# Optimization experiments

Measured on AMD Instinct MI355X. Metric: run time of the kernel, lower is better.

Reference implementation:

```python
import jax, jax.numpy as jnp
import numpy as np

DT = 0.02        # time step
DT_SKIP = DT * 20
ITERS = 49       # BDF2 iterations hardcoded in forward()
P = 64           # tronc (reduced dim)
NG_U = 8000      # HR sample count, u-equation
NG_V = 8000      # HR sample count, v-equation
B = 32           # batch of trajectories


def setup_inputs() -> dict:
    key = jax.random.key(0)
    k0, k1, k2, k3, k4 = jax.random.split(key, 5)
    state = jax.random.normal(k0, (B, P), dtype=jnp.float32)
    Ap = jax.random.normal(k1, (P, P), dtype=jnp.float32) * 0.05
    W_all_u = jax.random.normal(k2, (4 * NG_U, P), dtype=jnp.float32) * 0.02
    W_all_v = jax.random.normal(k3, (4 * NG_V, P), dtype=jnp.float32) * 0.02
    P_proj = jax.random.normal(k4, (P, NG_U + NG_V), dtype=jnp.float32) * 0.02
    return {"state": state, "Ap": Ap, "W_all_u": W_all_u,
            "W_all_v": W_all_v, "P_proj": P_proj}


def _rhs(a, W_all_u, W_all_v, P_proj):
    # a: (B, p) -> (B, p). Batched hyper-reduced quadratic RHS.
    zu = a @ W_all_u.T                       # (B, 4*Ng_u)
    uu, vu, dxu, dyu = jnp.split(zu, 4, axis=1)
    fu = uu * dxu + vu * dyu                 # (B, Ng_u)
    zv = a @ W_all_v.T                       # (B, 4*Ng_v)
    uv, vv, dxv, dyv = jnp.split(zv, 4, axis=1)
    fv = uv * dxv + vv * dyv                 # (B, Ng_v)
    concat = jnp.concatenate([fu, fv], axis=1)  # (B, Ng_u+Ng_v)
    return -(concat @ P_proj.T)              # (B, p)


def reference(state, Ap, W_all_u, W_all_v, P_proj):
    dt = jnp.float32(DT)
    a0 = state[:, :P]                        # state_rom (B, p)
    eye = jnp.eye(P, dtype=state.dtype)
    mat_1st = eye - dt * Ap[:P, :P]          # I - dt*A
    mat_2nd = 3.0 * eye - 2.0 * dt * Ap[:P, :P]

    # first step: implicit Euler
    f0 = _rhs(a0, W_all_u, W_all_v, P_proj)
    r0 = a0 + dt * f0
    a1 = jnp.linalg.solve(mat_1st, r0.T).T   # == lu_solve(LU_1st, ...)

    # BDF2 recurrence
    def step(carry, _):
        a_prev, f_prev, a_new = carry
        f_new = _rhs(a_new, W_all_u, W_all_v, P_proj)
        r = 4.0 * a_new - a_prev + 4.0 * dt * f_new - 2.0 * dt * f_prev
        a_next = jnp.linalg.solve(mat_2nd, r.T).T
        return (a_new, f_new, a_next), None

    (_, _, out_new), _ = jax.lax.scan(step, (a0, f0, a1), None, length=ITERS)
    return (out_new - a0) / jnp.float32(DT_SKIP)
```

## Files before the change

kernel.cpp:

```cpp
#include <hip/hip_runtime.h>

#define DTC 0.02f
#define INV_DT_SKIP 2.5f
#define NBLK 32
#define NSTEP 50

typedef __attribute__((ext_vector_type(8))) __bf16 bf16x8;
typedef __attribute__((ext_vector_type(4))) float f32x4;
typedef __attribute__((ext_vector_type(8))) unsigned short us8;
typedef unsigned long long u64t;

__device__ inline unsigned short f2bf(float x) {
    unsigned u = __float_as_uint(x);
    unsigned r = u + 0x7FFF + ((u >> 16) & 1u);
    return (unsigned short)(r >> 16);
}
__device__ inline float bf2f(unsigned short h) {
    return __uint_as_float(((unsigned)h) << 16);
}
__device__ inline unsigned pack2(float a, float b) {
    return (unsigned)f2bf(a) | ((unsigned)f2bf(b) << 16);
}
__device__ inline void gstore32(unsigned* p, unsigned v) {
    __hip_atomic_store(p, v, __ATOMIC_RELAXED, __HIP_MEMORY_SCOPE_AGENT);
}
__device__ inline u64t gload64(const u64t* p) {
    return __hip_atomic_load(p, __ATOMIC_RELAXED, __HIP_MEMORY_SCOPE_AGENT);
}

__global__ __launch_bounds__(256) void kinv(const float* __restrict__ Ap,
                                            float* __restrict__ inv1,
                                            float* __restrict__ inv2) {
    const int t = threadIdx.x;
    const float coef  = (blockIdx.x == 0) ? DTC : (2.0f * DTC / 3.0f);
    const float scale = (blockIdx.x == 0) ? 1.0f : (1.0f / 3.0f);
    float* outp = (blockIdx.x == 0) ? inv1 : inv2;

    __shared__ float ET[64 * 68];
    __shared__ float XA[64 * 68];
    __shared__ float XB[64 * 68];

    for (int idx = t; idx < 4096; idx += 256) {
        int r = idx >> 6, c = idx & 63;
        float e = coef * Ap[idx];
        ET[c * 68 + r] = e;
        XA[r * 68 + c] = ((r == c) ? 1.0f : 0.0f) + e;
    }
    __syncthreads();

    const int rr = (t >> 4) << 2;
    const int cc = (t & 15) << 2;
    float* bufs[2] = {XA, XB};
    for (int it = 0; it < 3; it++) {
        const float* Xin = bufs[it & 1];
        float* Xout = bufs[(it + 1) & 1];
        float acc[4][4];
        #pragma unroll
        for (int i = 0; i < 4; i++)
            #pragma unroll
            for (int j = 0; j < 4; j++)
                acc[i][j] = ((rr + i) == (cc + j)) ? 1.0f : 0.0f;
        for (int k = 0; k < 64; k++) {
            float4 e4 = *(const float4*)&ET[k * 68 + rr];
            float4 x4 = *(const float4*)&Xin[k * 68 + cc];
            float ev[4] = {e4.x, e4.y, e4.z, e4.w};
            float xv[4] = {x4.x, x4.y, x4.z, x4.w};
            #pragma unroll
            for (int i = 0; i < 4; i++)
                #pragma unroll
                for (int j = 0; j < 4; j++)
                    acc[i][j] += ev[i] * xv[j];
        }
        __syncthreads();
        #pragma unroll
        for (int i = 0; i < 4; i++)
            #pragma unroll
            for (int j = 0; j < 4; j++)
                Xout[(rr + i) * 68 + cc + j] = acc[i][j];
        __syncthreads();
    }
    const float* Xf = bufs[1];
    for (int idx = t; idx < 4096; idx += 256) {
        int r = idx >> 6, c = idx & 63;
        outp[idx] = scale * Xf[r * 68 + c];
    }
}

__global__ void kzero(unsigned* __restrict__ flags) {
    if (threadIdx.x < NBLK) flags[threadIdx.x] = 0u;
}

__device__ inline void flagbar(unsigned* flags, int blk, unsigned target) {
    __syncthreads();
    if (threadIdx.x < 64) {
        if (threadIdx.x == 0)
            __hip_atomic_store(&flags[blk], target, __ATOMIC_RELEASE, __HIP_MEMORY_SCOPE_AGENT);
        for (;;) {
            unsigned v = __hip_atomic_load(&flags[threadIdx.x & (NBLK - 1)], __ATOMIC_ACQUIRE,
                                           __HIP_MEMORY_SCOPE_AGENT);
            if (__all(v >= target)) break;
            __builtin_amdgcn_s_sleep(2);
        }
    }
    __syncthreads();
}

__global__ __launch_bounds__(512, 2)
void kmain(const float* __restrict__ state,
           const float* __restrict__ Wu,
           const float* __restrict__ Wv,
           const float* __restrict__ Pp,
           const float* __restrict__ inv1,
           const float* __restrict__ inv2,
           unsigned* __restrict__ pbuf,
           unsigned* __restrict__ flags,
           float* __restrict__ out) {
    const int t = threadIdx.x;
    const int l = t & 63;
    const int w = t >> 6;
    const int blk = blockIdx.x;
    const int gw = blk * 8 + w;
    const bool active = (gw < 250);

    __shared__ float Ab[3][2176];
    __shared__ float fb[8][16][36];
    __shared__ float red[8][1024];
    __shared__ float rbuf[32 * 68];

    for (int i = t; i < 2048; i += 512) Ab[0][(i >> 6) * 68 + (i & 63)] = state[i];
    if (!active)
        for (int i = l; i < 1024; i += 64) red[w][i] = 0.f;

    const int nr = l & 15;
    const int c0 = (l >> 4) << 3;
    const int cA = gw * 2;
    const float* W = (cA < 250) ? Wu : Wv;
    const int glA = ((cA < 250) ? cA : cA - 250) * 32;

    bf16x8 wf[2][2][4][2], pf[2][4], sfw[2];
    if (active) {
        #pragma unroll
        for (int ch = 0; ch < 2; ch++)
            #pragma unroll
            for (int th = 0; th < 2; th++)
                #pragma unroll
                for (int rb = 0; rb < 4; rb++)
                    #pragma unroll
                    for (int kt = 0; kt < 2; kt++) {
                        const float* s = W + (size_t)(rb * 8000 + glA + ch * 32 + th * 16 + nr) * 64
                                           + kt * 32 + c0;
                        us8 o;
                        #pragma unroll
                        for (int j = 0; j < 8; j++) o[j] = f2bf(s[j]);
                        wf[ch][th][rb][kt] = __builtin_bit_cast(bf16x8, o);
                    }
        #pragma unroll
        for (int ch = 0; ch < 2; ch++)
            #pragma unroll
            for (int pt = 0; pt < 4; pt++) {
                const float* s = Pp + (size_t)(pt * 16 + nr) * 16000 + (cA + ch) * 32 + c0;
                us8 o;
                #pragma unroll
                for (int j = 0; j < 8; j++) o[j] = f2bf(s[j]);
                pf[ch][pt] = __builtin_bit_cast(bf16x8, o);
            }
    }
    {
        const int ptS = w & 3;
        #pragma unroll
        for (int kt = 0; kt < 2; kt++) {
            int p = ptS * 16 + nr;
            const float* s = inv2 + (size_t)p * 64 + kt * 32 + c0;
            us8 o;
            #pragma unroll
            for (int j = 0; j < 8; j++) {
                float v = s[j] - ((p == kt * 32 + c0 + j) ? (1.0f / 3.0f) : 0.0f);
                o[j] = f2bf(v);
            }
            sfw[kt] = __builtin_bit_cast(bf16x8, o);
        }
    }
    __syncthreads();

    int ia_prev = 2, ia_cur = 0, ia_next = 1;
    float fprev[4];

    for (int k = 0; k < NSTEP; k++) {
        const int par = k & 1;
        unsigned* pslot = pbuf + (size_t)par * (NBLK * 1024) + blk * 1024;

        #pragma unroll
        for (int mt = 0; mt < 2; mt++) {
            if (active) {
                bf16x8 ahi[2], alo[2];
                {
                    const float* ac = Ab[ia_cur];
                    #pragma unroll
                    for (int kt = 0; kt < 2; kt++) {
                        us8 hv, lv;
                        #pragma unroll
                        for (int j = 0; j < 8; j++) {
                            float x = ac[(mt * 16 + nr) * 68 + kt * 32 + c0 + j];
                            unsigned short h = f2bf(x);
                            hv[j] = h;
                            lv[j] = f2bf(x - bf2f(h));
                        }
                        ahi[kt] = __builtin_bit_cast(bf16x8, hv);
                        alo[kt] = __builtin_bit_cast(bf16x8, lv);
                    }
                }
                const int col = l & 15, q4 = l >> 4;
                f32x4 racc[4] = {{0.f,0.f,0.f,0.f},{0.f,0.f,0.f,0.f},
                                 {0.f,0.f,0.f,0.f},{0.f,0.f,0.f,0.f}};
                #pragma unroll
                for (int ch = 0; ch < 2; ch++) {
                    #pragma unroll
                    for (int th = 0; th < 2; th++) {
                        f32x4 z[4];
                        #pragma unroll
                        for (int rb = 0; rb < 4; rb++) {
                            f32x4 acc = {0.f, 0.f, 0.f, 0.f};
                            #pragma unroll
                            for (int kt = 0; kt < 2; kt++) {
                                acc = __builtin_amdgcn_mfma_f32_16x16x32_bf16(ahi[kt], wf[ch][th][rb][kt], acc, 0, 0, 0);
                                acc = __builtin_amdgcn_mfma_f32_16x16x32_bf16(alo[kt], wf[ch][th][rb][kt], acc, 0, 0, 0);
                            }
                            z[rb] = acc;
                        }
                        #pragma unroll
                        for (int r = 0; r < 4; r++) {
                            float f = z[0][r] * z[2][r] + z[1][r] * z[3][r];
                            fb[w][q4 * 4 + r][th * 16 + col] = f;
                        }
                    }
                    bf16x8 ff;
                    {
                        us8 fv8;
                        #pragma unroll
                        for (int j = 0; j < 8; j++) fv8[j] = f2bf(fb[w][nr][c0 + j]);
                        ff = __builtin_bit_cast(bf16x8, fv8);
                    }
                    #pragma unroll
                    for (int pt = 0; pt < 4; pt++)
                        racc[pt] = __builtin_amdgcn_mfma_f32_16x16x32_bf16(ff, pf[ch][pt], racc[pt], 0, 0, 0);
                }
                #pragma unroll
                for (int pt = 0; pt < 4; pt++)
                    #pragma unroll
                    for (int r = 0; r < 4; r++)
                        red[w][(q4 * 4 + r) * 64 + pt * 16 + col] = racc[pt][r];
            }
            __syncthreads();
            {
                float s0 = 0.f, s1 = 0.f;
                #pragma unroll
                for (int w8 = 0; w8 < 8; w8++) {
                    s0 += red[w8][2 * t];
                    s1 += red[w8][2 * t + 1];
                }
                gstore32(&pslot[mt * 512 + t], pack2(s0, s1));
            }
            __syncthreads();
        }

        flagbar(flags, blk, (unsigned)(k + 1));

        float fv[4];
        {
            const u64t* pb = (const u64t*)(pbuf + (size_t)par * (NBLK * 1024));
            float s0 = 0.f, s1 = 0.f, s2 = 0.f, s3 = 0.f;
            #pragma unroll
            for (int s = 0; s < NBLK; s++) {
                u64t v = gload64(pb + (size_t)s * 512 + t);
                unsigned lo = (unsigned)v, hi = (unsigned)(v >> 32);
                s0 += __uint_as_float(lo << 16);
                s1 += __uint_as_float(lo & 0xffff0000u);
                s2 += __uint_as_float(hi << 16);
                s3 += __uint_as_float(hi & 0xffff0000u);
            }
            fv[0] = -s0; fv[1] = -s1; fv[2] = -s2; fv[3] = -s3;
        }

        {
            const int b = (4 * t) >> 6, p0 = (4 * t) & 63;
            #pragma unroll
            for (int jj = 0; jj < 4; jj++) {
                float f = fv[jj];
                int row = b * 68 + p0 + jj;
                float av = Ab[ia_cur][row];
                float rv = (k == 0) ? (av + DTC * f)
                                    : (4.f * av - Ab[ia_prev][row]
                                       + 4.f * DTC * f - 2.f * DTC * fprev[jj]);
                rbuf[row] = rv;
                fprev[jj] = f;
            }
        }
        __syncthreads();

        {
            const int mtS = w >> 2, ptS = w & 3;
            const int col = l & 15, q4 = l >> 4;
            bf16x8 S0, S1;
            float cb;
            if (k == 0) {
                #pragma unroll
                for (int kt = 0; kt < 2; kt++) {
                    int p = ptS * 16 + nr;
                    const float* s = inv1 + (size_t)p * 64 + kt * 32 + c0;
                    us8 o;
                    #pragma unroll
                    for (int j = 0; j < 8; j++) {
                        float v = s[j] - ((p == kt * 32 + c0 + j) ? 1.0f : 0.0f);
                        o[j] = f2bf(v);
                    }
                    if (kt == 0) S0 = __builtin_bit_cast(bf16x8, o);
                    else         S1 = __builtin_bit_cast(bf16x8, o);
                }
                cb = 1.0f;
            } else {
                S0 = sfw[0]; S1 = sfw[1];
                cb = 1.0f / 3.0f;
            }
            bf16x8 rhi[2], rlo[2];
            #pragma unroll
            for (int kt = 0; kt < 2; kt++) {
                us8 hv, lv;
                #pragma unroll
                for (int j = 0; j < 8; j++) {
                    float x = rbuf[(mtS * 16 + nr) * 68 + kt * 32 + c0 + j];
                    unsigned short h = f2bf(x);
                    hv[j] = h;
                    lv[j] = f2bf(x - bf2f(h));
                }
                rhi[kt] = __builtin_bit_cast(bf16x8, hv);
                rlo[kt] = __builtin_bit_cast(bf16x8, lv);
            }
            f32x4 acc;
            #pragma unroll
            for (int r = 0; r < 4; r++)
                acc[r] = rbuf[(mtS * 16 + q4 * 4 + r) * 68 + ptS * 16 + col] * cb;
            acc = __builtin_amdgcn_mfma_f32_16x16x32_bf16(rhi[0], S0, acc, 0, 0, 0);
            acc = __builtin_amdgcn_mfma_f32_16x16x32_bf16(rlo[0], S0, acc, 0, 0, 0);
            acc = __builtin_amdgcn_mfma_f32_16x16x32_bf16(rhi[1], S1, acc, 0, 0, 0);
            acc = __builtin_amdgcn_mfma_f32_16x16x32_bf16(rlo[1], S1, acc, 0, 0, 0);
            #pragma unroll
            for (int r = 0; r < 4; r++)
                Ab[ia_next][(mtS * 16 + q4 * 4 + r) * 68 + ptS * 16 + col] = acc[r];
        }
        __syncthreads();

        if (k == NSTEP - 1 && blk == 0) {
            for (int i = t; i < 2048; i += 512)
                out[i] = (Ab[ia_next][(i >> 6) * 68 + (i & 63)] - state[i]) * INV_DT_SKIP;
        }

        int tmp = ia_prev; ia_prev = ia_cur; ia_cur = ia_next; ia_next = tmp;
    }
}

extern "C" void kernel_launch(void* const* d_in, const int* in_sizes, int n_in,
                              void* d_out, int out_size, void* d_ws, size_t ws_size,
                              hipStream_t stream) {
    const float* state = (const float*)d_in[0];
    const float* Ap    = (const float*)d_in[1];
    const float* Wu    = (const float*)d_in[2];
    const float* Wv    = (const float*)d_in[3];
    const float* Pp    = (const float*)d_in[4];
    float* out = (float*)d_out;
    float* ws  = (float*)d_ws;

    float* inv1 = ws;
    float* inv2 = ws + 4096;
    unsigned* flags = (unsigned*)(ws + 8192);
    unsigned* pbuf  = (unsigned*)(ws + 8192 + 64);

    hipLaunchKernelGGL(kzero, dim3(1), dim3(64), 0, stream, flags);
    hipLaunchKernelGGL(kinv, dim3(2), dim3(256), 0, stream, Ap, inv1, inv2);
    hipLaunchKernelGGL(kmain, dim3(NBLK), dim3(512), 0, stream,
                       state, Wu, Wv, Pp, inv1, inv2, pbuf, flags, out);
}
```

Measured before the change: 613.1 us.

## Merge per-tile block barriers and replace flag barrier with relaxed all-wave polling

```diff
diff --git a/kernel.cpp b/kernel.cpp
--- a/kernel.cpp
+++ b/kernel.cpp
@@ -24,9 +24,13 @@
 __device__ inline void gstore32(unsigned* p, unsigned v) {
     __hip_atomic_store(p, v, __ATOMIC_RELAXED, __HIP_MEMORY_SCOPE_AGENT);
 }
+__device__ inline unsigned gload32(const unsigned* p) {
+    return __hip_atomic_load(p, __ATOMIC_RELAXED, __HIP_MEMORY_SCOPE_AGENT);
+}
 __device__ inline u64t gload64(const u64t* p) {
     return __hip_atomic_load(p, __ATOMIC_RELAXED, __HIP_MEMORY_SCOPE_AGENT);
 }
+#define PINV(x) asm volatile("" : "+v"(x))
 
 __global__ __launch_bounds__(256) void kinv(const float* __restrict__ Ap,
                                             float* __restrict__ inv1,
@@ -88,21 +92,6 @@
 
 __global__ void kzero(unsigned* __restrict__ flags) {
     if (threadIdx.x < NBLK) flags[threadIdx.x] = 0u;
-}
-
-__device__ inline void flagbar(unsigned* flags, int blk, unsigned target) {
-    __syncthreads();
-    if (threadIdx.x < 64) {
-        if (threadIdx.x == 0)
-            __hip_atomic_store(&flags[blk], target, __ATOMIC_RELEASE, __HIP_MEMORY_SCOPE_AGENT);
-        for (;;) {
-            unsigned v = __hip_atomic_load(&flags[threadIdx.x & (NBLK - 1)], __ATOMIC_ACQUIRE,
-                                           __HIP_MEMORY_SCOPE_AGENT);
-            if (__all(v >= target)) break;
-            __builtin_amdgcn_s_sleep(2);
-        }
-    }
-    __syncthreads();
 }
 
 __global__ __launch_bounds__(512, 2)
@@ -124,12 +113,13 @@
 
     __shared__ float Ab[3][2176];
     __shared__ float fb[8][16][36];
-    __shared__ float red[8][1024];
+    __shared__ float red2[2][8][1024];
     __shared__ float rbuf[32 * 68];
 
     for (int i = t; i < 2048; i += 512) Ab[0][(i >> 6) * 68 + (i & 63)] = state[i];
-    if (!active)
-        for (int i = l; i < 1024; i += 64) red[w][i] = 0.f;
+    if (!active) {
+        for (int i = l; i < 1024; i += 64) { red2[0][w][i] = 0.f; red2[1][w][i] = 0.f; }
+    }
 
     const int nr = l & 15;
     const int c0 = (l >> 4) << 3;
@@ -180,6 +170,18 @@
             sfw[kt] = __builtin_bit_cast(bf16x8, o);
         }
     }
+    #pragma unroll
+    for (int ch = 0; ch < 2; ch++) {
+        #pragma unroll
+        for (int th = 0; th < 2; th++)
+            #pragma unroll
+            for (int rb = 0; rb < 4; rb++)
+                #pragma unroll
+                for (int kt = 0; kt < 2; kt++) PINV(wf[ch][th][rb][kt]);
+        #pragma unroll
+        for (int pt = 0; pt < 4; pt++) PINV(pf[ch][pt]);
+    }
+    PINV(sfw[0]); PINV(sfw[1]);
     __syncthreads();
 
     int ia_prev = 2, ia_cur = 0, ia_next = 1;
@@ -189,9 +191,10 @@
         const int par = k & 1;
         unsigned* pslot = pbuf + (size_t)par * (NBLK * 1024) + blk * 1024;
 
-        #pragma unroll
-        for (int mt = 0; mt < 2; mt++) {
-            if (active) {
+        if (active) {
+            const int col = l & 15, q4 = l >> 4;
+            #pragma unroll
+            for (int mt = 0; mt < 2; mt++) {
                 bf16x8 ahi[2], alo[2];
                 {
                     const float* ac = Ab[ia_cur];
@@ -209,7 +212,6 @@
                         alo[kt] = __builtin_bit_cast(bf16x8, lv);
                     }
                 }
-                const int col = l & 15, q4 = l >> 4;
                 f32x4 racc[4] = {{0.f,0.f,0.f,0.f},{0.f,0.f,0.f,0.f},
                                  {0.f,0.f,0.f,0.f},{0.f,0.f,0.f,0.f}};
                 #pragma unroll
@@ -248,22 +250,33 @@
                 for (int pt = 0; pt < 4; pt++)
                     #pragma unroll
                     for (int r = 0; r < 4; r++)
-                        red[w][(q4 * 4 + r) * 64 + pt * 16 + col] = racc[pt][r];
-            }
-            __syncthreads();
-            {
-                float s0 = 0.f, s1 = 0.f;
-                #pragma unroll
-                for (int w8 = 0; w8 < 8; w8++) {
-                    s0 += red[w8][2 * t];
-                    s1 += red[w8][2 * t + 1];
-                }
-                gstore32(&pslot[mt * 512 + t], pack2(s0, s1));
-            }
-            __syncthreads();
-        }
-
-        flagbar(flags, blk, (unsigned)(k + 1));
+                        red2[mt][w][(q4 * 4 + r) * 64 + pt * 16 + col] = racc[pt][r];
+            }
+        }
+        __syncthreads();
+
+        #pragma unroll
+        for (int mt = 0; mt < 2; mt++) {
+            float s0 = 0.f, s1 = 0.f;
+            #pragma unroll
+            for (int w8 = 0; w8 < 8; w8++) {
+                s0 += red2[mt][w8][2 * t];
+                s1 += red2[mt][w8][2 * t + 1];
+            }
+            gstore32(&pslot[mt * 512 + t], pack2(s0, s1));
+        }
+        __syncthreads();
+
+        if (t == 0) gstore32(&flags[blk], (unsigned)(k + 1));
+        {
+            const unsigned target = (unsigned)(k + 1);
+            for (;;) {
+                unsigned v = gload32(&flags[l & (NBLK - 1)]);
+                if (__all(v >= target)) break;
+                __builtin_amdgcn_s_sleep(1);
+            }
+            asm volatile("" ::: "memory");
+        }
 
         float fv[4];
         {
```

New measurement: 544.9 us. 11.1% less time.
